# Performance work log

Hardware: AMD Instinct MI355X
Metric: run time of the kernel (lower is better)

## Reference

```python
import jax, jax.numpy as jnp
import numpy as np

B, S, D = 8, 4096, 256


def setup_inputs() -> dict:
    key = jax.random.key(0)
    kq, kk, kv, kb = jax.random.split(key, 4)
    q = jax.random.normal(kq, (B, S, D), dtype=jnp.float32)
    k = jax.random.normal(kk, (B, S, D), dtype=jnp.float32)
    v = jax.random.normal(kv, (B, S, D), dtype=jnp.float32)
    beta = jax.random.uniform(kb, (B, S), dtype=jnp.float32)
    return {"q": q, "k": k, "v": v, "beta": beta}


def reference(q, k, v, beta):
    # Delta-rule linear attention recurrence:
    #   h_t = beta_t * h_{t-1} + k_t^T v_t   (h: [B, D, D])
    #   o_t = q_t @ h_t                      (o: [B, D])
    dtype = q.dtype
    b, s, d = q.shape
    h0 = jnp.zeros((b, d, d), dtype=dtype)

    def step(h, inp):
        q_t, k_t, v_t, b_t = inp  # q_t/k_t/v_t: [B, D], b_t: [B]
        h = h * b_t[:, None, None] + jnp.einsum('bi,bj->bij', k_t, v_t)
        o_t = jnp.einsum('bi,bij->bj', q_t, h)
        return h, o_t

    xs = (q.transpose(1, 0, 2), k.transpose(1, 0, 2),
          v.transpose(1, 0, 2), beta.T)  # time-major
    _, out = jax.lax.scan(step, h0, xs)  # out: [S, B, D]
    return out.transpose(1, 0, 2)  # [B, S, D]
```

## Files before the change

### kernel.cpp

```cpp
#include <hip/hip_runtime.h>
#include <hip/hip_bf16.h>
#include <math.h>


#define B_ 8
#define S_ 4096
#define D_ 256
#define L_ 128
#define C_ (S_ / L_)
#define BC_ (B_ * C_)
#define STK 66

typedef __attribute__((ext_vector_type(8))) short s8v;
typedef __attribute__((ext_vector_type(4))) float f4v;
typedef unsigned short u16;
typedef unsigned int u32;

__device__ __forceinline__ u32 pk2(float lo, float hi) {
  union { __hip_bfloat162 h; u32 u; } cv;
  cv.h = __float22bfloat162_rn(make_float2(lo, hi));
  return cv.u;
}
__device__ __forceinline__ s8v pack8(const float4 a, const float4 b) {
  union { u32 u[4]; s8v v; } r;
  r.u[0] = pk2(a.x, a.y); r.u[1] = pk2(a.z, a.w);
  r.u[2] = pk2(b.x, b.y); r.u[3] = pk2(b.z, b.w);
  return r.v;
}

__global__ __launch_bounds__(512, 2) void ks_summary7(
    const float* __restrict__ kg, const float* __restrict__ vg,
    const float* __restrict__ beta, u16* __restrict__ A,
    float* __restrict__ P)
{
  __shared__ float ls[L_];
  __shared__ __align__(16) u16 U[2][256 * STK];
  __shared__ __align__(16) u16 BN[2][64 * 264];

  const int bc = blockIdx.x;
  const int b = bc / C_, c = bc % C_;
  const int tid = threadIdx.x;
  const float* betap = beta + (size_t)b * S_ + (size_t)c * L_;
  const float* kbase = kg + ((size_t)b * S_ + (size_t)c * L_) * D_;
  const float* vbase = vg + ((size_t)b * S_ + (size_t)c * L_) * D_;

  const int hh = tid >> 8;
  const int t2 = tid & 255;
  const int iLs = t2 & 7;
  const int s0s = (t2 >> 3) * 2;
  const int sg = hh * 64 + s0s;

  float bx0 = 1.f, bx1 = 1.f;
  if (tid < 64) { bx0 = betap[tid]; bx1 = betap[64 + tid]; }

  float4 kp[16], vp[16];
  {
    const float* k0 = kbase + (size_t)sg * D_;
    const float* v0 = vbase + (size_t)sg * D_;
#pragma unroll
    for (int p = 0; p < 8; ++p) {
      const int i0 = p * 32 + iLs * 4;
      kp[2 * p]     = *(const float4*)(k0 + i0);
      kp[2 * p + 1] = *(const float4*)(k0 + D_ + i0);
    }
#pragma unroll
    for (int p = 0; p < 8; ++p) {
      const int i0 = p * 32 + iLs * 4;
      vp[2 * p]     = *(const float4*)(v0 + i0);
      vp[2 * p + 1] = *(const float4*)(v0 + D_ + i0);
    }
  }

  if (tid < 64) {
    float x = log2f(fmaxf(bx0, 1e-30f));
#pragma unroll
    for (int off = 1; off < 64; off <<= 1) {
      float y = __shfl_up(x, off);
      if (tid >= off) x += y;
    }
    ls[tid] = x;
    const float tot0 = __shfl(x, 63);
    float z = log2f(fmaxf(bx1, 1e-30f));
#pragma unroll
    for (int off = 1; off < 64; off <<= 1) {
      float y = __shfl_up(z, off);
      if (tid >= off) z += y;
    }
    ls[64 + tid] = z + tot0;
  }
  __syncthreads();
  const float ltot = ls[L_ - 1];
  if (tid == 0) P[bc] = exp2f(ltot);

  {
    const float w0 = exp2f(ltot - ls[sg]);
    const float w1 = exp2f(ltot - ls[sg + 1]);
    u16* dst = U[hh];
#pragma unroll
    for (int p = 0; p < 8; ++p) {
      const int i0 = p * 32 + iLs * 4;
      const float4 a0 = kp[2 * p], a1 = kp[2 * p + 1];
      *(u32*)&dst[(i0 + 0) * STK + s0s] = pk2(a0.x * w0, a1.x * w1);
      *(u32*)&dst[(i0 + 1) * STK + s0s] = pk2(a0.y * w0, a1.y * w1);
      *(u32*)&dst[(i0 + 2) * STK + s0s] = pk2(a0.z * w0, a1.z * w1);
      *(u32*)&dst[(i0 + 3) * STK + s0s] = pk2(a0.w * w0, a1.w * w1);
    }
  }
  __syncthreads();

  const int lane = tid & 63, wave = tid >> 6;
  const int quad = lane >> 4, l15 = lane & 15;
  const int i0w = wave * 32;

  s8v af[2][4];
#pragma unroll
  for (int mt = 0; mt < 2; ++mt)
#pragma unroll
    for (int ks = 0; ks < 4; ++ks)
      af[mt][ks] = *(const s8v*)&U[ks >> 1][(i0w + mt * 16 + l15) * STK +
                                            (ks & 1) * 32 + quad * 8];
  __syncthreads();

  {
    u16* dst = U[hh];
#pragma unroll
    for (int p = 0; p < 8; ++p) {
      const int i0 = p * 32 + iLs * 4;
      const float4 a0 = vp[2 * p], a1 = vp[2 * p + 1];
      *(u32*)&dst[(i0 + 0) * STK + s0s] = pk2(a0.x, a1.x);
      *(u32*)&dst[(i0 + 1) * STK + s0s] = pk2(a0.y, a1.y);
      *(u32*)&dst[(i0 + 2) * STK + s0s] = pk2(a0.z, a1.z);
      *(u32*)&dst[(i0 + 3) * STK + s0s] = pk2(a0.w, a1.w);
    }
  }
  __syncthreads();

  u16* Ab = A + (size_t)bc * D_ * D_;

  for (int ng = 0; ng < 4; ++ng) {
    f4v acc[2][4];
#pragma unroll
    for (int mt = 0; mt < 2; ++mt)
#pragma unroll
      for (int nt = 0; nt < 4; ++nt) acc[mt][nt] = (f4v){0.f, 0.f, 0.f, 0.f};

#pragma unroll
    for (int ks = 0; ks < 4; ++ks) {
      const int so = (ks & 1) * 32 + quad * 8;
      s8v bv[4];
#pragma unroll
      for (int nt = 0; nt < 4; ++nt)
        bv[nt] = *(const s8v*)&U[ks >> 1][(ng * 64 + nt * 16 + l15) * STK + so];
#pragma unroll
      for (int mt = 0; mt < 2; ++mt)
#pragma unroll
        for (int nt = 0; nt < 4; ++nt)
          acc[mt][nt] = __builtin_amdgcn_mfma_f32_16x16x32_bf16(
              af[mt][ks], bv[nt], acc[mt][nt], 0, 0, 0);
    }
    u16* BNb = BN[ng & 1];
#pragma unroll
    for (int mt = 0; mt < 2; ++mt)
#pragma unroll
      for (int nt = 0; nt < 4; ++nt) {
        const int jl = nt * 16 + l15;
        uint2 w;
        w.x = pk2(acc[mt][nt][0], acc[mt][nt][1]);
        w.y = pk2(acc[mt][nt][2], acc[mt][nt][3]);
        *(uint2*)&BNb[jl * 264 + i0w + mt * 16 + quad * 4] = w;
      }
    __syncthreads();
    {
      const int jl = tid >> 3;
      const int il = (tid & 7) * 8;
#pragma unroll
      for (int p = 0; p < 4; ++p) {
        const int iu = il + p * 64;
        *(s8v*)&Ab[(size_t)(ng * 64 + jl) * D_ + iu] =
            *(const s8v*)&BNb[jl * 264 + iu];
      }
    }
  }
}

__global__ __launch_bounds__(256) void ks_scan7(
    u16* __restrict__ A, const float* __restrict__ P)
{
  const int g = blockIdx.x;
  const int b = g >> 6;
  const int unit = ((g & 63) << 8) + threadIdx.x;
  u16* base = A + (size_t)b * ((size_t)C_ * D_ * D_) + (size_t)unit * 4;
  const float* Pb = P + b * C_;

  uint2 d[C_];
#pragma unroll
  for (int c = 0; c < C_; ++c)
    d[c] = *(const uint2*)(base + (size_t)c * (D_ * D_));

  float h0 = 0.f, h1 = 0.f, h2 = 0.f, h3 = 0.f;
#pragma unroll
  for (int c = 0; c < C_; ++c) {
    const float pc = Pb[c];
    const uint2 u = d[c];
    const float a0 = __uint_as_float(u.x << 16);
    const float a1 = __uint_as_float(u.x & 0xFFFF0000u);
    const float a2 = __uint_as_float(u.y << 16);
    const float a3 = __uint_as_float(u.y & 0xFFFF0000u);
    d[c].x = pk2(h0, h1);
    d[c].y = pk2(h2, h3);
    h0 = fmaf(pc, h0, a0); h1 = fmaf(pc, h1, a1);
    h2 = fmaf(pc, h2, a2); h3 = fmaf(pc, h3, a3);
  }
#pragma unroll
  for (int c = 0; c < C_; ++c)
    *(uint2*)(base + (size_t)c * (D_ * D_)) = d[c];
}

__global__ __launch_bounds__(512, 2) void ks_output7(
    const float* __restrict__ qg, const float* __restrict__ kg,
    const float* __restrict__ vg, const float* __restrict__ beta,
    const u16* __restrict__ Hg, float* __restrict__ outg)
{
  __shared__ float ls[L_];
  __shared__ float cv[L_];
  __shared__ __align__(16) u16 QB[L_ * 264];
  __shared__ __align__(16) u16 Tm[L_ * 136];
  __shared__ __align__(16) u16 VT[256 * STK];

  const int bc = blockIdx.x;
  const int b = bc / C_, c = bc % C_;
  const int tid = threadIdx.x;
  const float* betap = beta + (size_t)b * S_ + (size_t)c * L_;
  const float* qbase = qg + ((size_t)b * S_ + (size_t)c * L_) * D_;
  const float* kbase = kg + ((size_t)b * S_ + (size_t)c * L_) * D_;
  const float* vbase = vg + ((size_t)b * S_ + (size_t)c * L_) * D_;
  const u16* Hb = Hg + (size_t)bc * D_ * D_;

  float bx0 = 1.f, bx1 = 1.f;
  if (tid < 64) { bx0 = betap[tid]; bx1 = betap[64 + tid]; }

  const int qt = tid >> 2, qc = (tid & 3) * 8;
  float4 qp[16];
  {
    const float* src = qbase + (size_t)qt * D_ + qc;
#pragma unroll
    for (int p = 0; p < 8; ++p) {
      qp[2 * p]     = *(const float4*)(src + p * 32);
      qp[2 * p + 1] = *(const float4*)(src + p * 32 + 4);
    }
  }
  const int iL3 = tid & 15;
  const int s03 = ((tid >> 4) & 31) * 2;
  float4 vp0[8];
  {
    const float* a0 = vbase + (size_t)s03 * D_;
#pragma unroll
    for (int p = 0; p < 4; ++p) {
      const int i0 = p * 64 + iL3 * 4;
      vp0[2 * p]     = *(const float4*)(a0 + i0);
      vp0[2 * p + 1] = *(const float4*)(a0 + D_ + i0);
    }
  }

  if (tid < 64) {
    float x = log2f(fmaxf(bx0, 1e-30f));
#pragma unroll
    for (int off = 1; off < 64; off <<= 1) {
      float y = __shfl_up(x, off);
      if (tid >= off) x += y;
    }
    ls[tid] = x;
    const float tot0 = __shfl(x, 63);
    float z = log2f(fmaxf(bx1, 1e-30f));
#pragma unroll
    for (int off = 1; off < 64; off <<= 1) {
      float y = __shfl_up(z, off);
      if (tid >= off) z += y;
    }
    ls[64 + tid] = z + tot0;
  }

#pragma unroll
  for (int p = 0; p < 8; ++p)
    *(s8v*)&QB[qt * 264 + qc + p * 32] = pack8(qp[2 * p], qp[2 * p + 1]);
  __syncthreads();
  if (tid < L_) cv[tid] = exp2f(ls[tid]);

  const int lane = tid & 63, wave = tid >> 6;
  const int quad = lane >> 4, l15 = lane & 15;
  const int j0w = wave * 32;

  {
    const int mA = wave * 16;
    f4v accA[8];
#pragma unroll
    for (int i = 0; i < 8; ++i) accA[i] = (f4v){0.f, 0.f, 0.f, 0.f};
#pragma unroll
    for (int kd = 0; kd < 8; ++kd) {
      const int d0 = kd * 32 + quad * 8;
      const float* krow = kbase + (size_t)(mA + l15) * D_ + d0;
      const s8v afr = pack8(*(const float4*)krow, *(const float4*)(krow + 4));
#pragma unroll
      for (int nt = 0; nt < 8; ++nt) {
        const s8v bf = *(const s8v*)&QB[(nt * 16 + l15) * 264 + d0];
        accA[nt] = __builtin_amdgcn_mfma_f32_16x16x32_bf16(afr, bf, accA[nt],
                                                           0, 0, 0);
      }
    }
#pragma unroll
    for (int nt = 0; nt < 8; ++nt) {
      const int t = nt * 16 + l15;
      const float lt = ls[t];
      const int s0 = mA + quad * 4;
      float v4[4];
#pragma unroll
      for (int r = 0; r < 4; ++r) {
        const int s = s0 + r;
        v4[r] = (s <= t) ? accA[nt][r] * exp2f(lt - ls[s]) : 0.f;
      }
      uint2 w;
      w.x = pk2(v4[0], v4[1]);
      w.y = pk2(v4[2], v4[3]);
      *(uint2*)&Tm[t * 136 + s0] = w;
    }
  }

  {
#pragma unroll
    for (int p = 0; p < 4; ++p) {
      const int i0 = p * 64 + iL3 * 4;
      const float4 a0 = vp0[2 * p], a1 = vp0[2 * p + 1];
      *(u32*)&VT[(i0 + 0) * STK + s03] = pk2(a0.x, a1.x);
      *(u32*)&VT[(i0 + 1) * STK + s03] = pk2(a0.y, a1.y);
      *(u32*)&VT[(i0 + 2) * STK + s03] = pk2(a0.z, a1.z);
      *(u32*)&VT[(i0 + 3) * STK + s03] = pk2(a0.w, a1.w);
    }
  }

  s8v hc[2];
#pragma unroll
  for (int mt = 0; mt < 2; ++mt)
    hc[mt] = *(const s8v*)(Hb + (size_t)(j0w + mt * 16 + l15) * D_ + quad * 8);

  __syncthreads();

  float4 vp1[8];
  {
    const float* b0 = vbase + (size_t)(64 + s03) * D_;
#pragma unroll
    for (int p = 0; p < 4; ++p) {
      const int i0 = p * 64 + iL3 * 4;
      vp1[2 * p]     = *(const float4*)(b0 + i0);
      vp1[2 * p + 1] = *(const float4*)(b0 + D_ + i0);
    }
  }

  f4v acc[2][8];
#pragma unroll
  for (int mt = 0; mt < 2; ++mt)
#pragma unroll
    for (int nt = 0; nt < 8; ++nt) acc[mt][nt] = (f4v){0.f, 0.f, 0.f, 0.f};

#pragma unroll
  for (int ks = 0; ks < 8; ++ks) {
    const int io = ks * 32 + quad * 8;
    s8v hn[2] = {hc[0], hc[1]};
    if (ks < 7) {
#pragma unroll
      for (int mt = 0; mt < 2; ++mt)
        hn[mt] = *(const s8v*)(Hb + (size_t)(j0w + mt * 16 + l15) * D_ +
                               io + 32);
    }
    s8v bfq[8];
#pragma unroll
    for (int nt = 0; nt < 8; ++nt)
      bfq[nt] = *(const s8v*)&QB[(nt * 16 + l15) * 264 + io];
#pragma unroll
    for (int mt = 0; mt < 2; ++mt)
#pragma unroll
      for (int nt = 0; nt < 8; ++nt)
        acc[mt][nt] = __builtin_amdgcn_mfma_f32_16x16x32_bf16(
            hc[mt], bfq[nt], acc[mt][nt], 0, 0, 0);
    hc[0] = hn[0]; hc[1] = hn[1];
  }
#pragma unroll
  for (int nt = 0; nt < 8; ++nt) {
    const float ct = cv[nt * 16 + l15];
#pragma unroll
    for (int mt = 0; mt < 2; ++mt) {
      acc[mt][nt][0] *= ct; acc[mt][nt][1] *= ct;
      acc[mt][nt][2] *= ct; acc[mt][nt][3] *= ct;
    }
  }

#pragma unroll
  for (int ks = 0; ks < 2; ++ks) {
    const int so = ks * 32 + quad * 8;
    s8v afv[2], bfv[8];
#pragma unroll
    for (int mt = 0; mt < 2; ++mt)
      afv[mt] = *(const s8v*)&VT[(j0w + mt * 16 + l15) * STK + so];
#pragma unroll
    for (int nt = 0; nt < 8; ++nt)
      bfv[nt] = *(const s8v*)&Tm[(nt * 16 + l15) * 136 + so];
#pragma unroll
    for (int mt = 0; mt < 2; ++mt)
#pragma unroll
      for (int nt = 0; nt < 8; ++nt)
        acc[mt][nt] = __builtin_amdgcn_mfma_f32_16x16x32_bf16(
            afv[mt], bfv[nt], acc[mt][nt], 0, 0, 0);
  }

  __syncthreads();
  {
#pragma unroll
    for (int p = 0; p < 4; ++p) {
      const int i0 = p * 64 + iL3 * 4;
      const float4 a0 = vp1[2 * p], a1 = vp1[2 * p + 1];
      *(u32*)&VT[(i0 + 0) * STK + s03] = pk2(a0.x, a1.x);
      *(u32*)&VT[(i0 + 1) * STK + s03] = pk2(a0.y, a1.y);
      *(u32*)&VT[(i0 + 2) * STK + s03] = pk2(a0.z, a1.z);
      *(u32*)&VT[(i0 + 3) * STK + s03] = pk2(a0.w, a1.w);
    }
  }
  __syncthreads();
#pragma unroll
  for (int ks = 0; ks < 2; ++ks) {
    const int so = ks * 32 + quad * 8;
    s8v afv[2], bfv[8];
#pragma unroll
    for (int mt = 0; mt < 2; ++mt)
      afv[mt] = *(const s8v*)&VT[(j0w + mt * 16 + l15) * STK + so];
#pragma unroll
    for (int nt = 0; nt < 8; ++nt)
      bfv[nt] = *(const s8v*)&Tm[(nt * 16 + l15) * 136 + 64 + so];
#pragma unroll
    for (int mt = 0; mt < 2; ++mt)
#pragma unroll
      for (int nt = 0; nt < 8; ++nt)
        acc[mt][nt] = __builtin_amdgcn_mfma_f32_16x16x32_bf16(
            afv[mt], bfv[nt], acc[mt][nt], 0, 0, 0);
  }

  float* ob = outg + ((size_t)b * S_ + (size_t)c * L_) * D_;
#pragma unroll
  for (int mt = 0; mt < 2; ++mt)
#pragma unroll
    for (int nt = 0; nt < 8; ++nt) {
      const int t = nt * 16 + l15;
      const int j0 = j0w + mt * 16 + quad * 4;
      float4 o;
      o.x = acc[mt][nt][0]; o.y = acc[mt][nt][1];
      o.z = acc[mt][nt][2]; o.w = acc[mt][nt][3];
      *(float4*)(ob + (size_t)t * D_ + j0) = o;
    }
}

extern "C" void kernel_launch(void* const* d_in, const int* in_sizes, int n_in,
                              void* d_out, int out_size, void* d_ws,
                              size_t ws_size, hipStream_t stream) {
  const float* q = (const float*)d_in[0];
  const float* k = (const float*)d_in[1];
  const float* v = (const float*)d_in[2];
  const float* beta = (const float*)d_in[3];
  float* out = (float*)d_out;

  u16* A = (u16*)d_ws;
  float* P = (float*)((char*)d_ws + (size_t)BC_ * D_ * D_ * sizeof(u16));

  ks_summary7<<<dim3(BC_), dim3(512), 0, stream>>>(k, v, beta, A, P);
  ks_scan7<<<dim3(512), dim3(256), 0, stream>>>(A, P);
  ks_output7<<<dim3(BC_), dim3(512), 0, stream>>>(q, k, v, beta, A, out);
}
```

Before: 172.0 us.

## Cut summary kernel registers and LDS, store MFMA results directly to global

The summary kernel drops its LDS transpose buffer and writes the bf16 MFMA accumulators straight to global memory, which removes a barrier per column group. The V prefetch is halved and the remaining half is loaded after the barrier, lowering register pressure so launch bounds can ask for four blocks per CU instead of two. The cost is narrower, less coalesced 8-byte global stores and some V load latency that is no longer hidden behind the beta scan.

```diff
diff --git a/kernel.cpp b/kernel.cpp
--- a/kernel.cpp
+++ b/kernel.cpp
@@ -28,14 +28,13 @@
   return r.v;
 }
 
-__global__ __launch_bounds__(512, 2) void ks_summary7(
+__global__ __launch_bounds__(512, 4) void ks_summary8(
     const float* __restrict__ kg, const float* __restrict__ vg,
     const float* __restrict__ beta, u16* __restrict__ A,
     float* __restrict__ P)
 {
   __shared__ float ls[L_];
   __shared__ __align__(16) u16 U[2][256 * STK];
-  __shared__ __align__(16) u16 BN[2][64 * 264];
 
   const int bc = blockIdx.x;
   const int b = bc / C_, c = bc % C_;
@@ -53,21 +52,14 @@
   float bx0 = 1.f, bx1 = 1.f;
   if (tid < 64) { bx0 = betap[tid]; bx1 = betap[64 + tid]; }
 
-  float4 kp[16], vp[16];
+  float4 kp[16];
   {
     const float* k0 = kbase + (size_t)sg * D_;
-    const float* v0 = vbase + (size_t)sg * D_;
 #pragma unroll
     for (int p = 0; p < 8; ++p) {
       const int i0 = p * 32 + iLs * 4;
       kp[2 * p]     = *(const float4*)(k0 + i0);
       kp[2 * p + 1] = *(const float4*)(k0 + D_ + i0);
-    }
-#pragma unroll
-    for (int p = 0; p < 8; ++p) {
-      const int i0 = p * 32 + iLs * 4;
-      vp[2 * p]     = *(const float4*)(v0 + i0);
-      vp[2 * p + 1] = *(const float4*)(v0 + D_ + i0);
     }
   }
 
@@ -112,6 +104,17 @@
   const int quad = lane >> 4, l15 = lane & 15;
   const int i0w = wave * 32;
 
+  float4 vb[8];
+  {
+    const float* v0 = vbase + (size_t)sg * D_;
+#pragma unroll
+    for (int p = 0; p < 4; ++p) {
+      const int i0 = p * 32 + iLs * 4;
+      vb[2 * p]     = *(const float4*)(v0 + i0);
+      vb[2 * p + 1] = *(const float4*)(v0 + D_ + i0);
+    }
+  }
+
   s8v af[2][4];
 #pragma unroll
   for (int mt = 0; mt < 2; ++mt)
@@ -124,14 +127,25 @@
   {
     u16* dst = U[hh];
 #pragma unroll
-    for (int p = 0; p < 8; ++p) {
+    for (int p = 0; p < 4; ++p) {
       const int i0 = p * 32 + iLs * 4;
-      const float4 a0 = vp[2 * p], a1 = vp[2 * p + 1];
+      const float4 a0 = vb[2 * p], a1 = vb[2 * p + 1];
       *(u32*)&dst[(i0 + 0) * STK + s0s] = pk2(a0.x, a1.x);
       *(u32*)&dst[(i0 + 1) * STK + s0s] = pk2(a0.y, a1.y);
       *(u32*)&dst[(i0 + 2) * STK + s0s] = pk2(a0.z, a1.z);
       *(u32*)&dst[(i0 + 3) * STK + s0s] = pk2(a0.w, a1.w);
     }
+    const float* v0 = vbase + (size_t)sg * D_;
+#pragma unroll
+    for (int p = 4; p < 8; ++p) {
+      const int i0 = p * 32 + iLs * 4;
+      const float4 a0 = *(const float4*)(v0 + i0);
+      const float4 a1 = *(const float4*)(v0 + D_ + i0);
+      *(u32*)&dst[(i0 + 0) * STK + s0s] = pk2(a0.x, a1.x);
+      *(u32*)&dst[(i0 + 1) * STK + s0s] = pk2(a0.y, a1.y);
+      *(u32*)&dst[(i0 + 2) * STK + s0s] = pk2(a0.z, a1.z);
+      *(u32*)&dst[(i0 + 3) * STK + s0s] = pk2(a0.w, a1.w);
+    }
   }
   __syncthreads();
 
@@ -158,32 +172,20 @@
           acc[mt][nt] = __builtin_amdgcn_mfma_f32_16x16x32_bf16(
               af[mt][ks], bv[nt], acc[mt][nt], 0, 0, 0);
     }
-    u16* BNb = BN[ng & 1];
 #pragma unroll
     for (int mt = 0; mt < 2; ++mt)
 #pragma unroll
       for (int nt = 0; nt < 4; ++nt) {
-        const int jl = nt * 16 + l15;
+        const int jl = ng * 64 + nt * 16 + l15;
         uint2 w;
         w.x = pk2(acc[mt][nt][0], acc[mt][nt][1]);
         w.y = pk2(acc[mt][nt][2], acc[mt][nt][3]);
-        *(uint2*)&BNb[jl * 264 + i0w + mt * 16 + quad * 4] = w;
+        *(uint2*)&Ab[(size_t)jl * D_ + i0w + mt * 16 + quad * 4] = w;
       }
-    __syncthreads();
-    {
-      const int jl = tid >> 3;
-      const int il = (tid & 7) * 8;
-#pragma unroll
-      for (int p = 0; p < 4; ++p) {
-        const int iu = il + p * 64;
-        *(s8v*)&Ab[(size_t)(ng * 64 + jl) * D_ + iu] =
-            *(const s8v*)&BNb[jl * 264 + iu];
-      }
-    }
-  }
-}
-
-__global__ __launch_bounds__(256) void ks_scan7(
+  }
+}
+
+__global__ __launch_bounds__(256) void ks_scan8(
     u16* __restrict__ A, const float* __restrict__ P)
 {
   const int g = blockIdx.x;
@@ -216,7 +218,7 @@
     *(uint2*)(base + (size_t)c * (D_ * D_)) = d[c];
 }
 
-__global__ __launch_bounds__(512, 2) void ks_output7(
+__global__ __launch_bounds__(512, 2) void ks_output8(
     const float* __restrict__ qg, const float* __restrict__ kg,
     const float* __restrict__ vg, const float* __restrict__ beta,
     const u16* __restrict__ Hg, float* __restrict__ outg)
@@ -468,7 +470,7 @@
   u16* A = (u16*)d_ws;
   float* P = (float*)((char*)d_ws + (size_t)BC_ * D_ * D_ * sizeof(u16));
 
-  ks_summary7<<<dim3(BC_), dim3(512), 0, stream>>>(k, v, beta, A, P);
-  ks_scan7<<<dim3(512), dim3(256), 0, stream>>>(A, P);
-  ks_output7<<<dim3(BC_), dim3(512), 0, stream>>>(q, k, v, beta, A, out);
-}
+  ks_summary8<<<dim3(BC_), dim3(512), 0, stream>>>(k, v, beta, A, P);
+  ks_scan8<<<dim3(512), dim3(256), 0, stream>>>(A, P);
+  ks_output8<<<dim3(BC_), dim3(512), 0, stream>>>(q, k, v, beta, A, out);
+}
```

Result: no change. 173.7 us (+1.0%).
